# Performance work log

Measured on AMD Instinct MI355X. Metric: run time of the kernel, lower is better.

The kernel has to match this reference:

```python
import jax, jax.numpy as jnp
import numpy as np

N_NODES = 100000   # number of graph nodes
N_EDGES = 1000000  # number of edges
D_IN = 64          # input feature dim
D_OUT = 64         # output feature dim
N_RELS = 16        # number of relation types


def setup_inputs() -> dict:
    key = jax.random.key(0)
    k1, k2, k3, k4, k5 = jax.random.split(key, 5)
    feat = jax.random.normal(k1, (N_NODES, D_IN), dtype=jnp.float32)
    weight = jax.random.normal(k2, (N_RELS, D_IN, D_OUT), dtype=jnp.float32) * 0.05
    src = jax.random.randint(k3, (N_EDGES,), 0, N_NODES)
    dst = jax.random.randint(k4, (N_EDGES,), 0, N_NODES)
    etypes = jax.random.randint(k5, (N_EDGES,), 0, N_RELS)
    return {"feat": feat, "weight": weight, "src": src, "dst": dst, "etypes": etypes}


def reference(feat, weight, src, dst, etypes):
    # gather source-node features per edge: h = edges.src['h']
    h = feat[src]                                # [E, d_in]
    n_rels = weight.shape[0]
    e, d_out = h.shape[0], weight.shape[2]

    # gather_mm(h, weight, idx_b=etypes): m_e = h_e @ weight[etypes_e]
    # grouped-GEMM realized as R masked dense GEMMs (R is small, fixed);
    # avoids materializing the [E, d_in, d_out] gathered weight tensor.
    def step(m, rw):
        r, w_r = rw
        mask = jnp.where(etypes == r, 1.0, 0.0).astype(h.dtype)  # [E]
        m = m + mask[:, None] * (h @ w_r)                        # [E, d_out]
        return m, None

    m0 = jnp.zeros((e, d_out), dtype=h.dtype)
    m, _ = jax.lax.scan(step, m0, (jnp.arange(n_rels), weight))

    # update_all(..., fn.sum('m', 'h')): scatter-sum messages to dst nodes
    out = jax.ops.segment_sum(m, dst, num_segments=feat.shape[0])  # [N, d_out]
    return out
```

## Files before the change

kernel.cpp:

```cpp
#include <hip/hip_runtime.h>
#include <hip/hip_bf16.h>
#include <stdint.h>

#define NNODES 100000
#define NEDGES 1000000
#define DIM 64
#define NRELS 16
#define EPB 2048
#define NB ((NEDGES + EPB - 1) / EPB)
#define PADCAP (NEDGES + NRELS * 64)
#define MAXTILES (PADCAP / 64)
#define NDN NNODES
#define BKT 256
#define NBKT ((NDN + BKT - 1) / BKT)

#define FEAT_BLKS 6250
#define W_BLKS 256
#define SETUP_BLKS (FEAT_BLKS + W_BLKS + NB)

#define WS_NEED 156943424ull

using short8  = __attribute__((ext_vector_type(8))) short;
using floatx4 = __attribute__((ext_vector_type(4))) float;
using uintx4  = __attribute__((ext_vector_type(4))) unsigned int;

__device__ __forceinline__ unsigned short f2bf(float f) {
    union { float f; uint32_t u; } v; v.f = f;
    uint32_t u = v.u;
    return (unsigned short)((u + 0x7FFFu + ((u >> 16) & 1u)) >> 16);
}
__device__ __forceinline__ float bf2f(uint32_t u16) {
    union { uint32_t u; float f; } v; v.u = u16 << 16;
    return v.f;
}
__device__ __forceinline__ uint32_t pk2(float a, float b) {
    __hip_bfloat162 h = __float22bfloat162_rn(make_float2(a, b));
    union { __hip_bfloat162 h; uint32_t u; } v; v.h = h;
    return v.u;
}

__global__ void k_setup(const float* __restrict__ feat, const float* __restrict__ W,
                        const int* __restrict__ et, const int* __restrict__ dst,
                        unsigned short* __restrict__ featB, unsigned short* __restrict__ Wt,
                        int* __restrict__ hist16, int* __restrict__ hist391) {
    __shared__ int cnt16[16];
    __shared__ int cnt391[NBKT];
    const int b = blockIdx.x;
    if (b < FEAT_BLKS) {
        int i = (b * 256 + threadIdx.x) * 4;
        const float4 f = *(const float4*)(feat + i);
        ushort4 o;
        o.x = f2bf(f.x); o.y = f2bf(f.y); o.z = f2bf(f.z); o.w = f2bf(f.w);
        *(ushort4*)(featB + i) = o;
    } else if (b < FEAT_BLKS + W_BLKS) {
        int t = (b - FEAT_BLKS) * 256 + threadIdx.x;
        int r = t >> 12, n = (t >> 6) & 63, k = t & 63;
        Wt[t] = f2bf(W[(r << 12) + (k << 6) + n]);
    } else {
        const int bb = b - (FEAT_BLKS + W_BLKS);
        if (threadIdx.x < 16) cnt16[threadIdx.x] = 0;
        for (int t = threadIdx.x; t < NBKT; t += 256) cnt391[t] = 0;
        __syncthreads();
        int start = bb * EPB;
        int end = min(NEDGES, start + EPB);
        for (int i = start + threadIdx.x; i < end; i += 256) {
            atomicAdd(&cnt16[et[i]], 1);
            atomicAdd(&cnt391[dst[i] >> 8], 1);
        }
        __syncthreads();
        if (threadIdx.x < 16) hist16[bb * 16 + threadIdx.x] = cnt16[threadIdx.x];
        for (int t = threadIdx.x; t < NBKT; t += 256)
            hist391[bb * NBKT + t] = cnt391[t];
    }
}

__global__ void k_scan(const int* __restrict__ hist, int* __restrict__ bbase,
                       int* __restrict__ Pve) {
    __shared__ int s_cnt[16];
    __shared__ int s_P[17];
    int w = threadIdx.x >> 6;
    int lane = threadIdx.x & 63;
    int carry = 0;
    for (int c = 0; c < NB; c += 64) {
        int idx = c + lane;
        int v = (idx < NB) ? hist[idx * 16 + w] : 0;
        int x = v;
        #pragma unroll
        for (int off = 1; off < 64; off <<= 1) {
            int y = __shfl_up(x, off);
            if (lane >= off) x += y;
        }
        if (idx < NB) bbase[idx * 16 + w] = carry + x - v;
        carry += __shfl(x, 63);
    }
    if (lane == 0) s_cnt[w] = carry;
    __syncthreads();
    if (threadIdx.x == 0) {
        int p = 0;
        for (int r = 0; r < 16; ++r) {
            s_P[r] = p;
            Pve[r] = p;
            Pve[17 + r] = p + s_cnt[r];
            p += (s_cnt[r] + 63) & ~63;
        }
        s_P[16] = p;
        Pve[16] = p;
    }
    __syncthreads();
    int pw = s_P[w];
    for (int idx = lane; idx < NB; idx += 64)
        bbase[idx * 16 + w] += pw;
}

__global__ void k_bscanA(const int* __restrict__ hist391, int* __restrict__ bbase391,
                         int* __restrict__ bstart) {
    int b = blockIdx.x * 4 + (threadIdx.x >> 6);
    int lane = threadIdx.x & 63;
    if (b >= NBKT) return;
    int carry = 0;
    for (int c = 0; c < NB; c += 64) {
        int idx = c + lane;
        int v = (idx < NB) ? hist391[idx * NBKT + b] : 0;
        int x = v;
        #pragma unroll
        for (int off = 1; off < 64; off <<= 1) {
            int y = __shfl_up(x, off);
            if (lane >= off) x += y;
        }
        if (idx < NB) bbase391[idx * NBKT + b] = carry + x - v;
        carry += __shfl(x, 63);
    }
    if (lane == 0) bstart[b] = carry;
}

__global__ void k_bscanB(int* __restrict__ bstart) {
    __shared__ int wtot[8];
    int t = threadIdx.x;
    int v = (t < NBKT) ? bstart[t] : 0;
    int lane = t & 63, w = t >> 6;
    int x = v;
    #pragma unroll
    for (int off = 1; off < 64; off <<= 1) {
        int y = __shfl_up(x, off);
        if (lane >= off) x += y;
    }
    if (lane == 63) wtot[w] = x;
    __syncthreads();
    int woff = 0;
    for (int i = 0; i < w; ++i) woff += wtot[i];
    if (t < NBKT) bstart[t] = woff + x - v;
    if (t == 511) {
        int total = 0;
        for (int i = 0; i < 8; ++i) total += wtot[i];
        bstart[NBKT] = total;
    }
}

__global__ void k_scatter(const int* __restrict__ et, const int* __restrict__ src,
                          const int* __restrict__ dst, const int* __restrict__ bbase16,
                          const int* __restrict__ bbase391, const int* __restrict__ bstart,
                          int2* __restrict__ pairE, unsigned short* __restrict__ dnode,
                          int buildPos) {
    __shared__ int base16[16];
    __shared__ int base391[NBKT];
    if (threadIdx.x < 16) base16[threadIdx.x] = bbase16[blockIdx.x * 16 + threadIdx.x];
    if (buildPos)
        for (int t = threadIdx.x; t < NBKT; t += 256)
            base391[t] = bbase391[blockIdx.x * NBKT + t] + bstart[t];
    __syncthreads();
    int start = blockIdx.x * EPB;
    int end = min(NEDGES, start + EPB);
    for (int i = start + threadIdx.x; i < end; i += 256) {
        int r = et[i];
        int pos = atomicAdd(&base16[r], 1);
        int d = dst[i];
        if (buildPos) {
            int bp = atomicAdd(&base391[d >> 8], 1);
            pairE[pos] = make_int2(src[i], bp);
            dnode[bp] = (unsigned short)(d & 255);
        } else {
            pairE[pos] = make_int2(src[i], d);
        }
    }
}

__global__ void __launch_bounds__(256)
k_bsort(const unsigned short* __restrict__ dnode, const int* __restrict__ bstart,
        int* __restrict__ remap, int* __restrict__ dnstart) {
    __shared__ int cnt[256];
    __shared__ int nodebase[256];
    __shared__ int wtot[4];
    const int b = blockIdx.x;
    const int start = bstart[b], end = bstart[b + 1];
    const int t = threadIdx.x;
    cnt[t] = 0;
    __syncthreads();
    for (int e = start + t; e < end; e += 256)
        atomicAdd(&cnt[dnode[e]], 1);
    __syncthreads();
    int v = cnt[t];
    int lane = t & 63, w = t >> 6;
    int x = v;
    #pragma unroll
    for (int off = 1; off < 64; off <<= 1) {
        int y = __shfl_up(x, off);
        if (lane >= off) x += y;
    }
    if (lane == 63) wtot[w] = x;
    __syncthreads();
    int woff = 0;
    for (int i = 0; i < w; ++i) woff += wtot[i];
    nodebase[t] = woff + x - v;
    cnt[t] = 0;
    __syncthreads();
    dnstart[b * 256 + t] = start + nodebase[t];
    if (b == NBKT - 1 && t == 255) dnstart[NBKT * 256] = end;
    for (int e = start + t; e < end; e += 256) {
        int node = dnode[e];
        int rk = atomicAdd(&cnt[node], 1);
        remap[e] = start + nodebase[node] + rk;
    }
}

__global__ void k_fix(int2* __restrict__ pairE, const int* __restrict__ remap) {
    int pos = blockIdx.x * 256 + threadIdx.x;
    if (pos >= PADCAP) return;
    int2 v = pairE[pos];
    v.y = ((unsigned)v.y < (unsigned)NEDGES) ? remap[v.y] : -1;
    pairE[pos] = v;
}

__global__ void __launch_bounds__(256)
k_computeA(const unsigned short* __restrict__ featB,
           const unsigned short* __restrict__ Wt,
           const int2* __restrict__ pairE, const int* __restrict__ Pve,
           unsigned short* __restrict__ msgE) {
    __shared__ float lds[4][16 * 68];
    const int w = threadIdx.x >> 6;
    const int t = blockIdx.x * 4 + w;
    const int base = t * 64;
    const int total = Pve[16];
    if (base >= total) return;
    int r = 0;
    while (base >= Pve[r + 1]) ++r;
    const int validEnd = Pve[17 + r];
    const int lane = threadIdx.x & 63;
    const int quad = lane >> 4;
    const int l16 = lane & 15;

    const unsigned short* wr = Wt + (r << 12);
    short8 bfr[4][2];
    #pragma unroll
    for (int tn = 0; tn < 4; ++tn)
        #pragma unroll
        for (int ks = 0; ks < 2; ++ks)
            bfr[tn][ks] = *(const short8*)(wr + ((tn * 16 + l16) << 6) + ks * 32 + quad * 8);

    const int rr = lane >> 2, seg = lane & 3;
    #pragma unroll
    for (int tm = 0; tm < 4; ++tm) {
        int row = base + tm * 16 + l16;
        int s = (row < validEnd) ? pairE[row].x : 0;
        const unsigned short* fp = featB + (s << 6) + quad * 8;
        short8 a0 = *(const short8*)(fp);
        short8 a1 = *(const short8*)(fp + 32);
        #pragma unroll
        for (int tn = 0; tn < 4; ++tn) {
            floatx4 c = {0.f, 0.f, 0.f, 0.f};
            c = __builtin_amdgcn_mfma_f32_16x16x32_bf16(a0, bfr[tn][0], c, 0, 0, 0);
            c = __builtin_amdgcn_mfma_f32_16x16x32_bf16(a1, bfr[tn][1], c, 0, 0, 0);
            #pragma unroll
            for (int j = 0; j < 4; ++j)
                lds[w][(quad * 4 + j) * 68 + tn * 16 + l16] = c[j];
        }
        int rowi = base + tm * 16 + rr;
        int p = (rowi < validEnd) ? pairE[rowi].y : -1;
        if (p >= 0) {
            const float* lp = &lds[w][rr * 68 + seg * 16];
            uintx4 o0, o1;
            o0.x = pk2(lp[0],  lp[1]);  o0.y = pk2(lp[2],  lp[3]);
            o0.z = pk2(lp[4],  lp[5]);  o0.w = pk2(lp[6],  lp[7]);
            o1.x = pk2(lp[8],  lp[9]);  o1.y = pk2(lp[10], lp[11]);
            o1.z = pk2(lp[12], lp[13]); o1.w = pk2(lp[14], lp[15]);
            uintx4* op = (uintx4*)(msgE + (size_t)p * 64 + seg * 16);
            __builtin_nontemporal_store(o0, op);
            __builtin_nontemporal_store(o1, op + 1);
        }
    }
}

__global__ void __launch_bounds__(256)
k_reduce(const unsigned short* __restrict__ msgE,
         const int* __restrict__ dnstart, float* __restrict__ out) {
    int n = blockIdx.x * 4 + (threadIdx.x >> 6);
    if (n >= NDN) return;
    int lane = threadIdx.x & 63;
    int start = dnstart[n];
    int end = dnstart[n + 1];
    int c8 = (lane & 7) * 8;
    float a0 = 0.f, a1 = 0.f, a2 = 0.f, a3 = 0.f;
    float a4 = 0.f, a5 = 0.f, a6 = 0.f, a7 = 0.f;
    for (int row = start + (lane >> 3); row < end; row += 8) {
        uintx4 v = *(const uintx4*)(msgE + (size_t)row * 64 + c8);
        a0 += bf2f(v.x & 0xffffu); a1 += bf2f(v.x >> 16);
        a2 += bf2f(v.y & 0xffffu); a3 += bf2f(v.y >> 16);
        a4 += bf2f(v.z & 0xffffu); a5 += bf2f(v.z >> 16);
        a6 += bf2f(v.w & 0xffffu); a7 += bf2f(v.w >> 16);
    }
    #pragma unroll
    for (int m = 8; m <= 32; m <<= 1) {
        a0 += __shfl_xor(a0, m); a1 += __shfl_xor(a1, m);
        a2 += __shfl_xor(a2, m); a3 += __shfl_xor(a3, m);
        a4 += __shfl_xor(a4, m); a5 += __shfl_xor(a5, m);
        a6 += __shfl_xor(a6, m); a7 += __shfl_xor(a7, m);
    }
    if (lane < 8) {
        float* op = out + (size_t)n * 64 + lane * 8;
        *(float4*)(op)     = make_float4(a0, a1, a2, a3);
        *(float4*)(op + 4) = make_float4(a4, a5, a6, a7);
    }
}

__global__ void __launch_bounds__(256)
k_compute(const unsigned short* __restrict__ featB,
          const unsigned short* __restrict__ Wt,
          const int2* __restrict__ pairE, const int* __restrict__ Pve,
          float* __restrict__ out) {
    const int t = blockIdx.x * 4 + (threadIdx.x >> 6);
    const int base = t * 64;
    const int total = Pve[16];
    if (base >= total) return;
    int r = 0;
    while (base >= Pve[r + 1]) ++r;
    const int validEnd = Pve[17 + r];
    const int lane = threadIdx.x & 63;
    const int quad = lane >> 4;
    const int l16 = lane & 15;

    const unsigned short* wr = Wt + (r << 12);
    short8 bfr[4][2];
    #pragma unroll
    for (int tn = 0; tn < 4; ++tn)
        #pragma unroll
        for (int ks = 0; ks < 2; ++ks)
            bfr[tn][ks] = *(const short8*)(wr + ((tn * 16 + l16) << 6) + ks * 32 + quad * 8);

    #pragma unroll
    for (int tm = 0; tm < 4; ++tm) {
        int row = base + tm * 16 + l16;
        int s = (row < validEnd) ? pairE[row].x : 0;
        const unsigned short* fp = featB + (s << 6) + quad * 8;
        short8 a0 = *(const short8*)(fp);
        short8 a1 = *(const short8*)(fp + 32);
        floatx4 cc[4];
        #pragma unroll
        for (int tn = 0; tn < 4; ++tn) {
            floatx4 c = {0.f, 0.f, 0.f, 0.f};
            c = __builtin_amdgcn_mfma_f32_16x16x32_bf16(a0, bfr[tn][0], c, 0, 0, 0);
            c = __builtin_amdgcn_mfma_f32_16x16x32_bf16(a1, bfr[tn][1], c, 0, 0, 0);
            cc[tn] = c;
        }
        int pos0 = base + tm * 16 + quad * 4;
        #pragma unroll
        for (int j = 0; j < 4; ++j) {
            if (pos0 + j < validEnd) {
                int dn = pairE[pos0 + j].y;
                float* op = out + (dn << 6) + l16;
                #pragma unroll
                for (int tn = 0; tn < 4; ++tn)
                    atomicAdd(op + tn * 16, cc[tn][j]);
            }
        }
    }
}

extern "C" void kernel_launch(void* const* d_in, const int* in_sizes, int n_in,
                              void* d_out, int out_size, void* d_ws, size_t ws_size,
                              hipStream_t stream) {
    const float* feat = (const float*)d_in[0];
    const float* W    = (const float*)d_in[1];
    const int* src    = (const int*)d_in[2];
    const int* dst    = (const int*)d_in[3];
    const int* et     = (const int*)d_in[4];
    float* out = (float*)d_out;
    char* ws = (char*)d_ws;

    unsigned short* featB = (unsigned short*)(ws);
    unsigned short* Wt    = (unsigned short*)(ws + 12800000);
    int* hist16   = (int*)(ws + 12931072);
    int* bbase16  = (int*)(ws + 12963840);
    int* Pve      = (int*)(ws + 12996608);
    int* hist391  = (int*)(ws + 12996864);
    int* bbase391 = (int*)(ws + 13764864);
    int* bstart   = (int*)(ws + 14532864);
    unsigned short* dnode = (unsigned short*)(ws + 14534464);
    int* dnstart  = (int*)(ws + 16534464);
    int* remap    = (int*)(ws + 16935232);
    int2* pairE   = (int2*)(ws + 20935232);
    unsigned short* msgE = (unsigned short*)(ws + 28943424);

    const int usePhases = (ws_size >= WS_NEED) ? 1 : 0;

    k_setup<<<SETUP_BLKS, 256, 0, stream>>>(feat, W, et, dst, featB, Wt, hist16, hist391);
    k_scan<<<1, 1024, 0, stream>>>(hist16, bbase16, Pve);

    if (usePhases) {
        k_bscanA<<<(NBKT + 3) / 4, 256, 0, stream>>>(hist391, bbase391, bstart);
        k_bscanB<<<1, 512, 0, stream>>>(bstart);
        k_scatter<<<NB, 256, 0, stream>>>(et, src, dst, bbase16, bbase391, bstart,
                                          pairE, dnode, 1);
        k_bsort<<<NBKT, 256, 0, stream>>>(dnode, bstart, remap, dnstart);
        k_fix<<<(PADCAP + 255) / 256, 256, 0, stream>>>(pairE, remap);
        k_computeA<<<(MAXTILES + 3) / 4, 256, 0, stream>>>(featB, Wt, pairE, Pve, msgE);
        k_reduce<<<(NDN + 3) / 4, 256, 0, stream>>>(msgE, dnstart, out);
    } else {
        hipMemsetAsync(d_out, 0, (size_t)out_size * sizeof(float), stream);
        k_scatter<<<NB, 256, 0, stream>>>(et, src, dst, bbase16, bbase391, bstart,
                                          pairE, dnode, 0);
        k_compute<<<(MAXTILES + 3) / 4, 256, 0, stream>>>(featB, Wt, pairE, Pve, out);
    }
}
```

Before: 251.9 us.

## Aggregate relation-count atomics per wavefront, merge scan kernels, use plain stores

The relation histogram and the scatter position assignment now use wavefront ballots, so one lane per relation issues a single aggregated LDS atomic instead of every lane contending on 16 counters. The relation scan and the per-bucket scan are fused into one launch, with block 0 doing the relation scan and the other blocks doing bucket columns, which removes a kernel launch. Message stores in the compute kernel change from nontemporal to ordinary stores, so the messages may stay in cache for the reduce pass. The ballot loop adds 16 ballots per element, and the fused kernel now also runs the bucket scans in the fallback path, where that work is unused.

Result: no change. 249.1 us (-1.1%).

```diff
diff --git a/kernel.cpp b/kernel.cpp
--- a/kernel.cpp
+++ b/kernel.cpp
@@ -17,6 +17,7 @@
 #define FEAT_BLKS 6250
 #define W_BLKS 256
 #define SETUP_BLKS (FEAT_BLKS + W_BLKS + NB)
+#define SCANS_BLKS (1 + (NBKT + 15) / 16)
 
 #define WS_NEED 156943424ull
 
@@ -64,7 +65,14 @@
         int start = bb * EPB;
         int end = min(NEDGES, start + EPB);
         for (int i = start + threadIdx.x; i < end; i += 256) {
-            atomicAdd(&cnt16[et[i]], 1);
+            int r = et[i];
+            int lid = threadIdx.x & 63;
+            #pragma unroll
+            for (int rel = 0; rel < 16; ++rel) {
+                unsigned long long m = __ballot(r == rel);
+                if (r == rel && lid == __ffsll((long long)m) - 1)
+                    atomicAdd(&cnt16[rel], __popcll(m));
+            }
             atomicAdd(&cnt391[dst[i] >> 8], 1);
         }
         __syncthreads();
@@ -74,63 +82,64 @@
     }
 }
 
-__global__ void k_scan(const int* __restrict__ hist, int* __restrict__ bbase,
-                       int* __restrict__ Pve) {
-    __shared__ int s_cnt[16];
-    __shared__ int s_P[17];
+__global__ void __launch_bounds__(1024)
+k_scans(const int* __restrict__ hist16, int* __restrict__ bbase16,
+        int* __restrict__ Pve,
+        const int* __restrict__ hist391, int* __restrict__ bbase391,
+        int* __restrict__ bstart) {
     int w = threadIdx.x >> 6;
     int lane = threadIdx.x & 63;
-    int carry = 0;
-    for (int c = 0; c < NB; c += 64) {
-        int idx = c + lane;
-        int v = (idx < NB) ? hist[idx * 16 + w] : 0;
-        int x = v;
-        #pragma unroll
-        for (int off = 1; off < 64; off <<= 1) {
-            int y = __shfl_up(x, off);
-            if (lane >= off) x += y;
-        }
-        if (idx < NB) bbase[idx * 16 + w] = carry + x - v;
-        carry += __shfl(x, 63);
-    }
-    if (lane == 0) s_cnt[w] = carry;
-    __syncthreads();
-    if (threadIdx.x == 0) {
-        int p = 0;
-        for (int r = 0; r < 16; ++r) {
-            s_P[r] = p;
-            Pve[r] = p;
-            Pve[17 + r] = p + s_cnt[r];
-            p += (s_cnt[r] + 63) & ~63;
-        }
-        s_P[16] = p;
-        Pve[16] = p;
-    }
-    __syncthreads();
-    int pw = s_P[w];
-    for (int idx = lane; idx < NB; idx += 64)
-        bbase[idx * 16 + w] += pw;
-}
-
-__global__ void k_bscanA(const int* __restrict__ hist391, int* __restrict__ bbase391,
-                         int* __restrict__ bstart) {
-    int b = blockIdx.x * 4 + (threadIdx.x >> 6);
-    int lane = threadIdx.x & 63;
-    if (b >= NBKT) return;
-    int carry = 0;
-    for (int c = 0; c < NB; c += 64) {
-        int idx = c + lane;
-        int v = (idx < NB) ? hist391[idx * NBKT + b] : 0;
-        int x = v;
-        #pragma unroll
-        for (int off = 1; off < 64; off <<= 1) {
-            int y = __shfl_up(x, off);
-            if (lane >= off) x += y;
-        }
-        if (idx < NB) bbase391[idx * NBKT + b] = carry + x - v;
-        carry += __shfl(x, 63);
-    }
-    if (lane == 0) bstart[b] = carry;
+    if (blockIdx.x == 0) {
+        __shared__ int s_cnt[16];
+        __shared__ int s_P[17];
+        int carry = 0;
+        for (int c = 0; c < NB; c += 64) {
+            int idx = c + lane;
+            int v = (idx < NB) ? hist16[idx * 16 + w] : 0;
+            int x = v;
+            #pragma unroll
+            for (int off = 1; off < 64; off <<= 1) {
+                int y = __shfl_up(x, off);
+                if (lane >= off) x += y;
+            }
+            if (idx < NB) bbase16[idx * 16 + w] = carry + x - v;
+            carry += __shfl(x, 63);
+        }
+        if (lane == 0) s_cnt[w] = carry;
+        __syncthreads();
+        if (threadIdx.x == 0) {
+            int p = 0;
+            for (int r = 0; r < 16; ++r) {
+                s_P[r] = p;
+                Pve[r] = p;
+                Pve[17 + r] = p + s_cnt[r];
+                p += (s_cnt[r] + 63) & ~63;
+            }
+            s_P[16] = p;
+            Pve[16] = p;
+        }
+        __syncthreads();
+        int pw = s_P[w];
+        for (int idx = lane; idx < NB; idx += 64)
+            bbase16[idx * 16 + w] += pw;
+    } else {
+        int b = (blockIdx.x - 1) * 16 + w;
+        if (b >= NBKT) return;
+        int carry = 0;
+        for (int c = 0; c < NB; c += 64) {
+            int idx = c + lane;
+            int v = (idx < NB) ? hist391[idx * NBKT + b] : 0;
+            int x = v;
+            #pragma unroll
+            for (int off = 1; off < 64; off <<= 1) {
+                int y = __shfl_up(x, off);
+                if (lane >= off) x += y;
+            }
+            if (idx < NB) bbase391[idx * NBKT + b] = carry + x - v;
+            carry += __shfl(x, 63);
+        }
+        if (lane == 0) bstart[b] = carry;
+    }
 }
 
 __global__ void k_bscanB(int* __restrict__ bstart) {
@@ -172,7 +181,19 @@
     int end = min(NEDGES, start + EPB);
     for (int i = start + threadIdx.x; i < end; i += 256) {
         int r = et[i];
-        int pos = atomicAdd(&base16[r], 1);
+        int lid = threadIdx.x & 63;
+        unsigned long long same = 0;
+        #pragma unroll
+        for (int rel = 0; rel < 16; ++rel) {
+            unsigned long long m = __ballot(r == rel);
+            if (r == rel) same = m;
+        }
+        int leader = __ffsll((long long)same) - 1;
+        int rank = __popcll(same & ((1ull << lid) - 1ull));
+        int base;
+        if (lid == leader) base = atomicAdd(&base16[r], __popcll(same));
+        base = __shfl(base, leader);
+        int pos = base + rank;
         int d = dst[i];
         if (buildPos) {
             int bp = atomicAdd(&base391[d >> 8], 1);
@@ -283,8 +304,8 @@
             o1.x = pk2(lp[8],  lp[9]);  o1.y = pk2(lp[10], lp[11]);
             o1.z = pk2(lp[12], lp[13]); o1.w = pk2(lp[14], lp[15]);
             uintx4* op = (uintx4*)(msgE + (size_t)p * 64 + seg * 16);
-            __builtin_nontemporal_store(o0, op);
-            __builtin_nontemporal_store(o1, op + 1);
+            op[0] = o0;
+            op[1] = o1;
         }
     }
 }
@@ -402,10 +423,10 @@
     const int usePhases = (ws_size >= WS_NEED) ? 1 : 0;
 
     k_setup<<<SETUP_BLKS, 256, 0, stream>>>(feat, W, et, dst, featB, Wt, hist16, hist391);
-    k_scan<<<1, 1024, 0, stream>>>(hist16, bbase16, Pve);
+    k_scans<<<SCANS_BLKS, 1024, 0, stream>>>(hist16, bbase16, Pve, hist391,
+                                             bbase391, bstart);
 
     if (usePhases) {
-        k_bscanA<<<(NBKT + 3) / 4, 256, 0, stream>>>(hist391, bbase391, bstart);
         k_bscanB<<<1, 512, 0, stream>>>(bstart);
         k_scatter<<<NB, 256, 0, stream>>>(et, src, dst, bbase16, bbase391, bstart,
                                           pairE, dnode, 1);
```
